# Kernel tuning notes

Measured on AMD Instinct MI355X. Metric: run time of the kernel, lower is better.

## Reference

```python
import jax, jax.numpy as jnp
import numpy as np

D_MODEL = 1024
N_HEADS = 16
D_K = D_MODEL // N_HEADS
B, T = 2, 2048


def setup_inputs() -> dict:
    key = jax.random.key(0)
    ks = jax.random.split(key, 12)
    s = 0.02
    return {
        "q": jax.random.normal(ks[0], (B, T, D_MODEL), jnp.float32),
        "k": jax.random.normal(ks[1], (B, T, D_MODEL), jnp.float32),
        "v": jax.random.normal(ks[2], (B, T, D_MODEL), jnp.float32),
        "Wq": jax.random.normal(ks[3], (D_MODEL, D_MODEL), jnp.float32) * s,
        "bq": jnp.zeros((D_MODEL,), jnp.float32),
        "Wk": jax.random.normal(ks[4], (D_MODEL, D_MODEL), jnp.float32) * s,
        "bk": jnp.zeros((D_MODEL,), jnp.float32),
        "Wv": jax.random.normal(ks[5], (D_MODEL, D_MODEL), jnp.float32) * s,
        "bv": jnp.zeros((D_MODEL,), jnp.float32),
        "Wo": jax.random.normal(ks[6], (D_MODEL, D_MODEL), jnp.float32) * s,
        "bo": jnp.zeros((D_MODEL,), jnp.float32),
        "mask": jnp.ones((B, T), jnp.int32),
        "causal": 1,
    }


def reference(q, k, v, Wq, bq, Wk, bk, Wv, bv, Wo, bo, mask, causal):
    Bq, Tq, D = q.shape
    Tk = k.shape[1]
    # projections (torch Linear: x @ W.T + b), split heads -> [B, H, T, d_k]
    qh = (q @ Wq.T + bq).reshape(Bq, Tq, N_HEADS, D_K).transpose(0, 2, 1, 3)
    kh = (k @ Wk.T + bk).reshape(Bq, Tk, N_HEADS, D_K).transpose(0, 2, 1, 3)
    vh = (v @ Wv.T + bv).reshape(Bq, Tk, N_HEADS, D_K).transpose(0, 2, 1, 3)
    scores = jnp.einsum("bhqd,bhkd->bhqk", qh, kh) / jnp.sqrt(jnp.float32(D_K))
    neg_inf = jnp.float32(-jnp.inf)
    if mask is not None:
        scores = jnp.where(mask[:, None, None, :] == 0, neg_inf, scores)
    if causal:
        causal_mask = jnp.tril(jnp.ones((Tq, Tq), jnp.float32))
        scores = jnp.where(causal_mask == 0, neg_inf, scores)
    attn = jax.nn.softmax(scores, axis=-1)
    out = jnp.einsum("bhqk,bhkd->bhqd", attn, vh)
    out = out.transpose(0, 2, 1, 3).reshape(Bq, Tq, D)
    return out @ Wo.T + bo
```

## Files before the change

### kernel.cpp

```cpp
#include <hip/hip_runtime.h>
#include <cstdint>
#include <cstddef>


typedef __bf16 bf16x8 __attribute__((ext_vector_type(8)));
typedef float f32x4 __attribute__((ext_vector_type(4)));

#define MFMA(a, b, c) __builtin_amdgcn_mfma_f32_16x16x32_bf16((a), (b), (c), 0, 0, 0)

static constexpr int D_MODEL = 1024;
static constexpr int T_ = 2048;
static constexpr int M_TOK = 4096;

__device__ __forceinline__ unsigned short f32_to_bf16(float f) {
    union { float f; uint32_t u; } v; v.f = f;
    uint32_t u = v.u;
    uint32_t r = u + 0x7fffu + ((u >> 16) & 1u);
    return (unsigned short)(r >> 16);
}
__device__ __forceinline__ unsigned f32_to_bf16_fast(float f) {
    union { float f; uint32_t u; } v; v.f = f;
    return (v.u + 0x8000u) >> 16;
}

typedef __attribute__((address_space(1))) void* as1_ptr;
typedef __attribute__((address_space(3))) void* as3_ptr;
__device__ __forceinline__ void gload_lds16(const void* g, void* l) {
    __builtin_amdgcn_global_load_lds((as1_ptr)(void*)g, (as3_ptr)l, 16, 0, 0);
}

__device__ __forceinline__ int keyperm(int k) {
    return (k & 32) | ((k & 12) << 1) | ((k & 16) >> 2) | (k & 3);
}

__global__ __launch_bounds__(256) void cvt_all(
    const float* __restrict__ q, const float* __restrict__ k,
    const float* __restrict__ v, const float* __restrict__ wq,
    const float* __restrict__ wk, const float* __restrict__ wv,
    const float* __restrict__ wo, ushort4* __restrict__ dst) {
    int i = blockIdx.x * blockDim.x + threadIdx.x;
    constexpr int R = 1 << 20;
    const float* s;
    int idx;
    if (i < 3 * R) {
        s = (i < R) ? q : (i < 2 * R) ? k : v;
        idx = i & (R - 1);
    } else {
        int j = i - 3 * R;
        int w = j >> 18;
        s = (w == 0) ? wq : (w == 1) ? wk : (w == 2) ? wv : wo;
        idx = j & ((1 << 18) - 1);
    }
    float4 f = ((const float4*)s)[idx];
    ushort4 o;
    o.x = (unsigned short)f32_to_bf16(f.x); o.y = (unsigned short)f32_to_bf16(f.y);
    o.z = (unsigned short)f32_to_bf16(f.z); o.w = (unsigned short)f32_to_bf16(f.w);
    dst[i] = o;
}

template<int MODE, int NT16>
__device__ __forceinline__ void gemm_body(
    const unsigned short* __restrict__ A, const unsigned short* __restrict__ W,
    const float* __restrict__ bias, void* __restrict__ outp,
    unsigned short* As, unsigned short* Ws, int bx, int by)
{
    constexpr bool SWAP = (MODE != 2);
    const int tid = threadIdx.x;
    const int lane = tid & 63, wave = tid >> 6;
    const int wm = wave >> 1, wn = wave & 1;
    const int r16 = lane & 15, kg = lane >> 4;
    const int m_blk = by * 128, n_blk = bx * (NT16 * 32);

    f32x4 acc[4][NT16];
    #pragma unroll
    for (int mt = 0; mt < 4; ++mt)
        #pragma unroll
        for (int nt = 0; nt < NT16; ++nt) acc[mt][nt] = (f32x4){0, 0, 0, 0};

    for (int k0 = 0; k0 < D_MODEL; k0 += 64) {
        __syncthreads();
        #pragma unroll
        for (int j = 0; j < 4; ++j) {
            int si = j * 256 + tid;
            int row = si >> 3, cg = (si & 7) ^ (row & 7);
            gload_lds16(A + (size_t)(m_blk + row) * D_MODEL + k0 + cg * 8,
                        (char*)As + (j * 256 + wave * 64) * 16);
        }
        #pragma unroll
        for (int j = 0; j < NT16; ++j) {
            int si = j * 256 + tid;
            int row = si >> 3, cg = (si & 7) ^ (row & 7);
            gload_lds16(W + (size_t)(n_blk + row) * D_MODEL + k0 + cg * 8,
                        (char*)Ws + (j * 256 + wave * 64) * 16);
        }
        __syncthreads();
        #pragma unroll
        for (int kc = 0; kc < 2; ++kc) {
            bf16x8 af[4], wf[NT16];
            #pragma unroll
            for (int mt = 0; mt < 4; ++mt) {
                int row = wm * 64 + mt * 16 + r16;
                af[mt] = *(const bf16x8*)(As + row * 64 + (((kc * 4 + kg) ^ (row & 7)) * 8));
            }
            #pragma unroll
            for (int nt = 0; nt < NT16; ++nt) {
                int row = wn * (NT16 * 16) + nt * 16 + r16;
                wf[nt] = *(const bf16x8*)(Ws + row * 64 + (((kc * 4 + kg) ^ (row & 7)) * 8));
            }
            #pragma unroll
            for (int mt = 0; mt < 4; ++mt)
                #pragma unroll
                for (int nt = 0; nt < NT16; ++nt)
                    acc[mt][nt] = SWAP ? MFMA(wf[nt], af[mt], acc[mt][nt])
                                       : MFMA(af[mt], wf[nt], acc[mt][nt]);
        }
    }
    if (MODE == 2) {
        #pragma unroll
        for (int nt = 0; nt < NT16; ++nt) {
            int n = n_blk + wn * (NT16 * 16) + nt * 16 + r16;
            float bn = bias[n];
            int hh = n >> 6, dki = n & 63;
            #pragma unroll
            for (int mt = 0; mt < 4; ++mt) {
                int m0 = m_blk + wm * 64 + mt * 16 + kg * 4;
                int mp = (m0 & ~63) | keyperm(m0 & 63);
                int bb = mp >> 11, ti = mp & 2047;
                ushort4 pk;
                pk.x = f32_to_bf16(acc[mt][nt][0] + bn);
                pk.y = f32_to_bf16(acc[mt][nt][1] + bn);
                pk.z = f32_to_bf16(acc[mt][nt][2] + bn);
                pk.w = f32_to_bf16(acc[mt][nt][3] + bn);
                *(ushort4*)((unsigned short*)outp +
                    ((size_t)(bb * 16 + hh) * 64 + dki) * 2048 + ti) = pk;
            }
        }
    } else {
        #pragma unroll
        for (int nt = 0; nt < NT16; ++nt) {
            int n0 = n_blk + wn * (NT16 * 16) + nt * 16 + kg * 4;
            float4 bn4 = *(const float4*)(bias + n0);
            #pragma unroll
            for (int mt = 0; mt < 4; ++mt) {
                int m = m_blk + wm * 64 + mt * 16 + r16;
                if (MODE == 3) {
                    float4 st;
                    st.x = acc[mt][nt][0] + bn4.x; st.y = acc[mt][nt][1] + bn4.y;
                    st.z = acc[mt][nt][2] + bn4.z; st.w = acc[mt][nt][3] + bn4.w;
                    *(float4*)((float*)outp + (size_t)m * D_MODEL + n0) = st;
                } else {
                    ushort4 pk;
                    pk.x = f32_to_bf16(acc[mt][nt][0] + bn4.x);
                    pk.y = f32_to_bf16(acc[mt][nt][1] + bn4.y);
                    pk.z = f32_to_bf16(acc[mt][nt][2] + bn4.z);
                    pk.w = f32_to_bf16(acc[mt][nt][3] + bn4.w);
                    *(ushort4*)((unsigned short*)outp + (size_t)m * D_MODEL + n0) = pk;
                }
            }
        }
    }
}

__global__ __launch_bounds__(256) void gemm_qkv(
    const unsigned short* __restrict__ qb, const unsigned short* __restrict__ kb,
    const unsigned short* __restrict__ vb, const unsigned short* __restrict__ Wqb,
    const unsigned short* __restrict__ Wkb, const unsigned short* __restrict__ Wvb,
    const float* __restrict__ bq, const float* __restrict__ bk, const float* __restrict__ bv,
    unsigned short* __restrict__ Qhp, unsigned short* __restrict__ Khp,
    unsigned short* __restrict__ Vtp)
{
    __shared__ __align__(16) unsigned short As[128 * 64];
    __shared__ __align__(16) unsigned short Ws[128 * 64];
    const int z = blockIdx.z;
    const unsigned short* A = (z == 0) ? qb : (z == 1) ? kb : vb;
    const unsigned short* W = (z == 0) ? Wqb : (z == 1) ? Wkb : Wvb;
    const float* bias = (z == 0) ? bq : (z == 1) ? bk : bv;
    if (z < 2)
        gemm_body<0, 4>(A, W, bias, (z == 0) ? (void*)Qhp : (void*)Khp, As, Ws,
                        blockIdx.x, blockIdx.y);
    else
        gemm_body<2, 4>(A, W, bias, (void*)Vtp, As, Ws, blockIdx.x, blockIdx.y);
}

__global__ __launch_bounds__(256) void gemm_out(
    const unsigned short* __restrict__ ab, const unsigned short* __restrict__ Wob,
    const float* __restrict__ bo, float* __restrict__ outp)
{
    __shared__ __align__(16) unsigned short As[128 * 64];
    __shared__ __align__(16) unsigned short Ws[64 * 64];
    gemm_body<3, 2>(ab, Wob, bo, (void*)outp, As, Ws, blockIdx.x, blockIdx.y);
}

__global__ __launch_bounds__(256) void attn_fwd(
    const unsigned short* __restrict__ Qh, const unsigned short* __restrict__ Kh,
    const unsigned short* __restrict__ Vt, const int* __restrict__ mask,
    const int* __restrict__ causal_p, unsigned short* __restrict__ attnout)
{
    __shared__ __align__(16) unsigned short Ks[2][64 * 64];
    __shared__ __align__(16) unsigned short Vs[2][64 * 64];

    const int tid = threadIdx.x;
    const int lane = tid & 63, wave = tid >> 6;
    const int bh = blockIdx.x;
    const int y = blockIdx.y, y0 = y & 7, j4 = y >> 3;
    const int qc = (j4 == 0) ? y0 : (j4 == 1) ? (15 - y0)
                 : (j4 == 2) ? (16 + y0) : (31 - y0);
    const int b = bh >> 4, h = bh & 15;
    const int causal = *causal_p;
    const int r16 = lane & 15, kg = lane >> 4;

    const int q0 = qc * 64 + wave * 16;

    const unsigned short* Qb = Qh + (size_t)b * T_ * D_MODEL + h * 64;
    const unsigned short* Kb = Kh + (size_t)b * T_ * D_MODEL + h * 64;
    const unsigned short* Vb = Vt + (size_t)bh * 64 * T_;
    const int* mb = mask + b * T_;

    bf16x8 qf0 = *(const bf16x8*)(Qb + (size_t)(q0 + r16) * D_MODEL + kg * 8);
    bf16x8 qf1 = *(const bf16x8*)(Qb + (size_t)(q0 + r16) * D_MODEL + 32 + kg * 8);

    float l = 0.f;
    f32x4 o[4];
    #pragma unroll
    for (int f = 0; f < 4; ++f) o[f] = (f32x4){0, 0, 0, 0};
    const float sc2 = 0.18033688011112042f;
    const int lim = wave * 16 + r16;

    const int nT = causal ? (qc + 1) : 32;

    auto stage = [&](int buf, int t) {
        int t0 = t * 64;
        #pragma unroll
        for (int j = 0; j < 2; ++j) {
            int si = j * 256 + tid;
            int row = si >> 3, cg = (si & 7) ^ (row & 7);
            gload_lds16(Kb + (size_t)(t0 + row) * D_MODEL + cg * 8,
                        (char*)Ks[buf] + (j * 256 + wave * 64) * 16);
            gload_lds16(Vb + (size_t)row * T_ + t0 + cg * 8,
                        (char*)Vs[buf] + (j * 256 + wave * 64) * 16);
        }
    };

    stage(0, 0);
    for (int t = 0; t < nT; ++t) {
        __syncthreads();
        if (t + 1 < nT) stage((t + 1) & 1, t + 1);
        const unsigned short* Kst = Ks[t & 1];
        const unsigned short* Vst = Vs[t & 1];
        const int t0 = t * 64;
        const bool diag = causal && (t == qc);

        unsigned long long km = __ballot(mb[t0 + lane] != 0);

        f32x4 s[4];
        #pragma unroll
        for (int c = 0; c < 4; ++c) {
            int key = c * 16 + r16;
            bf16x8 kf0 = *(const bf16x8*)(Kst + key * 64 + ((kg ^ (key & 7)) * 8));
            bf16x8 kf1 = *(const bf16x8*)(Kst + key * 64 + (((4 + kg) ^ (key & 7)) * 8));
            f32x4 z = (f32x4){0, 0, 0, 0};
            z = MFMA(kf0, qf0, z);
            z = MFMA(kf1, qf1, z);
            s[c] = z;
        }

        float pv[4][4];
        if (!diag && km == ~0ull) {
            #pragma unroll
            for (int c = 0; c < 4; ++c)
                #pragma unroll
                for (int r = 0; r < 4; ++r) {
                    float e = __builtin_amdgcn_exp2f(s[c][r] * sc2);
                    pv[c][r] = e; l += e;
                }
        } else {
            #pragma unroll
            for (int c = 0; c < 4; ++c) {
                unsigned mc = (unsigned)(km >> (c * 16));
                #pragma unroll
                for (int r = 0; r < 4; ++r) {
                    int kbit = kg * 4 + r;
                    bool ok = ((mc >> kbit) & 1) && (!diag || (c * 16 + kbit <= lim));
                    float e = ok ? __builtin_amdgcn_exp2f(s[c][r] * sc2) : 0.f;
                    pv[c][r] = e; l += e;
                }
            }
        }

        union pk_t { unsigned u[4]; bf16x8 v; };
        pk_t pa[2];
        #pragma unroll
        for (int c = 0; c < 4; ++c) {
            int half = (c & 1) * 2;
            pa[c >> 1].u[half]     = f32_to_bf16_fast(pv[c][0]) | (f32_to_bf16_fast(pv[c][1]) << 16);
            pa[c >> 1].u[half + 1] = f32_to_bf16_fast(pv[c][2]) | (f32_to_bf16_fast(pv[c][3]) << 16);
        }

        #pragma unroll
        for (int f = 0; f < 4; ++f) {
            int row = f * 16 + r16;
            int rx = row & 7;
            #pragma unroll
            for (int cp = 0; cp < 2; ++cp) {
                int g = cp * 4 + kg;
                bf16x8 vf = *(const bf16x8*)(Vst + row * 64 + ((g ^ rx) * 8));
                o[f] = MFMA(pa[cp].v, vf, o[f]);
            }
        }
    }

    l += __shfl_xor(l, 16, 64); l += __shfl_xor(l, 32, 64);
    float inv = (l > 0.f) ? 1.0f / l : 0.f;
    #pragma unroll
    for (int r = 0; r < 4; ++r) {
        int ql = kg * 4 + r;
        float iv = __shfl(inv, ql, 64);
        size_t base = ((size_t)(b * T_ + q0 + ql)) * D_MODEL + h * 64;
        #pragma unroll
        for (int f = 0; f < 4; ++f)
            attnout[base + f * 16 + r16] = f32_to_bf16(o[f][r] * iv);
    }
}

extern "C" void kernel_launch(void* const* d_in, const int* in_sizes, int n_in,
                              void* d_out, int out_size, void* d_ws, size_t ws_size,
                              hipStream_t stream) {
    const float* q  = (const float*)d_in[0];
    const float* k  = (const float*)d_in[1];
    const float* v  = (const float*)d_in[2];
    const float* Wq = (const float*)d_in[3];
    const float* bq = (const float*)d_in[4];
    const float* Wk = (const float*)d_in[5];
    const float* bk = (const float*)d_in[6];
    const float* Wv = (const float*)d_in[7];
    const float* bv = (const float*)d_in[8];
    const float* Wo = (const float*)d_in[9];
    const float* bo = (const float*)d_in[10];
    const int* mask   = (const int*)d_in[11];
    const int* causal = (const int*)d_in[12];

    const size_t SZ_TOK = (size_t)M_TOK * D_MODEL;
    const size_t SZ_W   = (size_t)D_MODEL * D_MODEL;

    unsigned short* qb  = (unsigned short*)d_ws;
    unsigned short* kb  = qb  + SZ_TOK;
    unsigned short* vb  = kb  + SZ_TOK;
    unsigned short* Wqb = vb  + SZ_TOK;
    unsigned short* Wkb = Wqb + SZ_W;
    unsigned short* Wvb = Wkb + SZ_W;
    unsigned short* Wob = Wvb + SZ_W;
    unsigned short* Qhp = Wob + SZ_W;
    unsigned short* Khp = Qhp + SZ_TOK;
    unsigned short* Vtp = Khp + SZ_TOK;
    unsigned short* ab  = Vtp + SZ_TOK;

    cvt_all<<<16384, 256, 0, stream>>>(q, k, v, Wq, Wk, Wv, Wo, (ushort4*)qb);

    gemm_qkv<<<dim3(D_MODEL / 128, M_TOK / 128, 3), 256, 0, stream>>>(
        qb, kb, vb, Wqb, Wkb, Wvb, bq, bk, bv, Qhp, Khp, Vtp);

    attn_fwd<<<dim3(32, 32), 256, 0, stream>>>(Qhp, Khp, Vtp, mask, causal, ab);

    gemm_out<<<dim3(D_MODEL / 64, M_TOK / 128), 256, 0, stream>>>(ab, Wob, bo,
                                                                  (float*)d_out);
}
```

Measured before the change: 226.0 us.

## Double-buffer GEMM LDS tiles, swizzle block order, precompute attention key masks

The GEMM main loop now double-buffers the A and W shared-memory tiles, issuing the next k-slice's global-to-LDS loads before computing on the current one, and drops one barrier per iteration. Global and LDS addresses are hoisted out of the loop. Both GEMM kernels remap block indices so that neighbouring blocks share A and W rows for better L2 locality. The attention kernel builds all per-tile key-mask ballots once into shared memory instead of loading the mask every iteration. Doubling LDS per block may lower occupancy, and the single barrier per iteration relies on the load-completion waits inside the helper.

```diff
diff --git a/kernel.cpp b/kernel.cpp
--- a/kernel.cpp
+++ b/kernel.cpp
@@ -65,47 +65,65 @@
     unsigned short* As, unsigned short* Ws, int bx, int by)
 {
     constexpr bool SWAP = (MODE != 2);
+    constexpr int ASZ = 128 * 64;
+    constexpr int WSZ = NT16 * 32 * 64;
     const int tid = threadIdx.x;
     const int lane = tid & 63, wave = tid >> 6;
     const int wm = wave >> 1, wn = wave & 1;
     const int r16 = lane & 15, kg = lane >> 4;
     const int m_blk = by * 128, n_blk = bx * (NT16 * 32);
 
+    const unsigned short* Ap[4]; unsigned short* Al[4];
+    #pragma unroll
+    for (int j = 0; j < 4; ++j) {
+        int si = j * 256 + tid;
+        int row = si >> 3, cg = (si & 7) ^ (row & 7);
+        Ap[j] = A + (size_t)(m_blk + row) * D_MODEL + cg * 8;
+        Al[j] = As + (j * 256 + wave * 64) * 8;
+    }
+    const unsigned short* Wp[NT16]; unsigned short* Wl[NT16];
+    #pragma unroll
+    for (int j = 0; j < NT16; ++j) {
+        int si = j * 256 + tid;
+        int row = si >> 3, cg = (si & 7) ^ (row & 7);
+        Wp[j] = W + (size_t)(n_blk + row) * D_MODEL + cg * 8;
+        Wl[j] = Ws + (j * 256 + wave * 64) * 8;
+    }
+
     f32x4 acc[4][NT16];
     #pragma unroll
     for (int mt = 0; mt < 4; ++mt)
         #pragma unroll
         for (int nt = 0; nt < NT16; ++nt) acc[mt][nt] = (f32x4){0, 0, 0, 0};
 
-    for (int k0 = 0; k0 < D_MODEL; k0 += 64) {
+    auto stage = [&](int bb, int k0) {
+        #pragma unroll
+        for (int j = 0; j < 4; ++j)
+            gload_lds16(Ap[j] + k0, Al[j] + bb * ASZ);
+        #pragma unroll
+        for (int j = 0; j < NT16; ++j)
+            gload_lds16(Wp[j] + k0, Wl[j] + bb * WSZ);
+    };
+
+    constexpr int NKS = D_MODEL / 64;
+    stage(0, 0);
+    for (int ks = 0; ks < NKS; ++ks) {
         __syncthreads();
-        #pragma unroll
-        for (int j = 0; j < 4; ++j) {
-            int si = j * 256 + tid;
-            int row = si >> 3, cg = (si & 7) ^ (row & 7);
-            gload_lds16(A + (size_t)(m_blk + row) * D_MODEL + k0 + cg * 8,
-                        (char*)As + (j * 256 + wave * 64) * 16);
-        }
-        #pragma unroll
-        for (int j = 0; j < NT16; ++j) {
-            int si = j * 256 + tid;
-            int row = si >> 3, cg = (si & 7) ^ (row & 7);
-            gload_lds16(W + (size_t)(n_blk + row) * D_MODEL + k0 + cg * 8,
-                        (char*)Ws + (j * 256 + wave * 64) * 16);
-        }
-        __syncthreads();
+        if (ks + 1 < NKS) stage((ks + 1) & 1, (ks + 1) * 64);
+        const unsigned short* Asb = As + (ks & 1) * ASZ;
+        const unsigned short* Wsb = Ws + (ks & 1) * WSZ;
         #pragma unroll
         for (int kc = 0; kc < 2; ++kc) {
             bf16x8 af[4], wf[NT16];
             #pragma unroll
             for (int mt = 0; mt < 4; ++mt) {
                 int row = wm * 64 + mt * 16 + r16;
-                af[mt] = *(const bf16x8*)(As + row * 64 + (((kc * 4 + kg) ^ (row & 7)) * 8));
+                af[mt] = *(const bf16x8*)(Asb + row * 64 + (((kc * 4 + kg) ^ (row & 7)) * 8));
             }
             #pragma unroll
             for (int nt = 0; nt < NT16; ++nt) {
                 int row = wn * (NT16 * 16) + nt * 16 + r16;
-                wf[nt] = *(const bf16x8*)(Ws + row * 64 + (((kc * 4 + kg) ^ (row & 7)) * 8));
+                wf[nt] = *(const bf16x8*)(Wsb + row * 64 + (((kc * 4 + kg) ^ (row & 7)) * 8));
             }
             #pragma unroll
             for (int mt = 0; mt < 4; ++mt)
@@ -169,26 +187,31 @@
     unsigned short* __restrict__ Qhp, unsigned short* __restrict__ Khp,
     unsigned short* __restrict__ Vtp)
 {
-    __shared__ __align__(16) unsigned short As[128 * 64];
-    __shared__ __align__(16) unsigned short Ws[128 * 64];
-    const int z = blockIdx.z;
+    __shared__ __align__(16) unsigned short As[2 * 128 * 64];
+    __shared__ __align__(16) unsigned short Ws[2 * 128 * 64];
+    int flat = blockIdx.x + (blockIdx.y << 3) + (blockIdx.z << 8);
+    int w = (flat & 7) * 96 + (flat >> 3);
+    int bx = w & 7, by = (w >> 3) & 31, z = w >> 8;
     const unsigned short* A = (z == 0) ? qb : (z == 1) ? kb : vb;
     const unsigned short* W = (z == 0) ? Wqb : (z == 1) ? Wkb : Wvb;
     const float* bias = (z == 0) ? bq : (z == 1) ? bk : bv;
     if (z < 2)
         gemm_body<0, 4>(A, W, bias, (z == 0) ? (void*)Qhp : (void*)Khp, As, Ws,
-                        blockIdx.x, blockIdx.y);
+                        bx, by);
     else
-        gemm_body<2, 4>(A, W, bias, (void*)Vtp, As, Ws, blockIdx.x, blockIdx.y);
+        gemm_body<2, 4>(A, W, bias, (void*)Vtp, As, Ws, bx, by);
 }
 
 __global__ __launch_bounds__(256) void gemm_out(
     const unsigned short* __restrict__ ab, const unsigned short* __restrict__ Wob,
     const float* __restrict__ bo, float* __restrict__ outp)
 {
-    __shared__ __align__(16) unsigned short As[128 * 64];
-    __shared__ __align__(16) unsigned short Ws[64 * 64];
-    gemm_body<3, 2>(ab, Wob, bo, (void*)outp, As, Ws, blockIdx.x, blockIdx.y);
+    __shared__ __align__(16) unsigned short As[2 * 128 * 64];
+    __shared__ __align__(16) unsigned short Ws[2 * 64 * 64];
+    int flat = blockIdx.x + (blockIdx.y << 4);
+    int w = (flat & 7) * 64 + (flat >> 3);
+    int bx = w & 15, by = w >> 4;
+    gemm_body<3, 2>(ab, Wob, bo, (void*)outp, As, Ws, bx, by);
 }
 
 __global__ __launch_bounds__(256) void attn_fwd(
@@ -198,6 +221,7 @@
 {
     __shared__ __align__(16) unsigned short Ks[2][64 * 64];
     __shared__ __align__(16) unsigned short Vs[2][64 * 64];
+    __shared__ unsigned long long kmS[32];
 
     const int tid = threadIdx.x;
     const int lane = tid & 63, wave = tid >> 6;
@@ -216,6 +240,12 @@
     const unsigned short* Vb = Vt + (size_t)bh * 64 * T_;
     const int* mb = mask + b * T_;
 
+    #pragma unroll
+    for (int t = wave; t < 32; t += 4) {
+        unsigned long long m = __ballot(mb[t * 64 + lane] != 0);
+        if (lane == 0) kmS[t] = m;
+    }
+
     bf16x8 qf0 = *(const bf16x8*)(Qb + (size_t)(q0 + r16) * D_MODEL + kg * 8);
     bf16x8 qf1 = *(const bf16x8*)(Qb + (size_t)(q0 + r16) * D_MODEL + 32 + kg * 8);
 
@@ -247,10 +277,9 @@
         if (t + 1 < nT) stage((t + 1) & 1, t + 1);
         const unsigned short* Kst = Ks[t & 1];
         const unsigned short* Vst = Vs[t & 1];
-        const int t0 = t * 64;
         const bool diag = causal && (t == qc);
 
-        unsigned long long km = __ballot(mb[t0 + lane] != 0);
+        unsigned long long km = kmS[t];
 
         f32x4 s[4];
         #pragma unroll
```

After: 222.9 us. About the same (-1.4%).
